# Kernel optimization log

Hardware: AMD Instinct MI355X
Metric: run time of the kernel (lower is better)

Reference implementation:

```python
import jax, jax.numpy as jnp
import numpy as np

B, GH, GW = 8, 32, 32
S = GH * GW            # 1024
HIDDEN = 512
D = 64                 # head_dim
NUM_HOPS = 2
EPS = 1e-6


def setup_inputs() -> dict:
    key = jax.random.key(0)
    ks = jax.random.split(key, 8)

    def init(k, shape, std):
        return (jax.random.normal(k, shape) * std).astype(jnp.float32)

    x = jax.random.normal(ks[0], (B, S, HIDDEN), dtype=jnp.float32)
    Wq = init(ks[1], (D, HIDDEN), HIDDEN ** -0.5)
    Wk = init(ks[2], (D, HIDDEN), HIDDEN ** -0.5)
    Wv = init(ks[3], (D, HIDDEN), HIDDEN ** -0.5)
    bias_table = init(ks[4], (2 * GH - 1, 2 * GW - 1), 0.02)
    fusion_w = jnp.ones((NUM_HOPS, 3), dtype=jnp.float32)
    fusion_b = jnp.zeros((NUM_HOPS,), dtype=jnp.float32)
    hop_W = init(ks[5], (NUM_HOPS, D, D), D ** -0.5)
    gate_W = init(ks[6], (NUM_HOPS, HIDDEN), HIDDEN ** -0.5)
    gate_b = jnp.zeros((NUM_HOPS,), dtype=jnp.float32)
    out_W = init(ks[7], (HIDDEN, D), D ** -0.5)
    temperature = jnp.ones((1,), dtype=jnp.float32)

    # relative position index [S, S] (buffer, constant)
    coords = np.stack(np.meshgrid(np.arange(GH), np.arange(GW), indexing='ij')).reshape(2, -1)
    rel = coords[:, :, None] - coords[:, None, :]
    rel[0] += GH - 1
    rel[1] += GW - 1
    rel_idx = jnp.asarray(rel[0] * (2 * GW - 1) + rel[1], dtype=jnp.int32)

    return dict(x=x, Wq=Wq, Wk=Wk, Wv=Wv, bias_table=bias_table,
                fusion_w=fusion_w, fusion_b=fusion_b, hop_W=hop_W,
                gate_W=gate_W, gate_b=gate_b, out_W=out_W,
                temperature=temperature, rel_idx=rel_idx)


def _rotate_half(u):
    d = u.shape[-1] // 2
    return jnp.concatenate([-u[..., d:], u[..., :d]], axis=-1)


def _prob_log(p):
    p = jnp.clip(p, EPS, 1.0 - EPS)
    return jnp.log(p / (1.0 - p + EPS))


def _mat_exp(M, h):
    R = M
    for _ in range(h - 1):
        R = jnp.matmul(R, M)
    return R


def _row_norm(M):
    return M / (jnp.sum(M, axis=-1, keepdims=True) + EPS)


def reference(x, Wq, Wk, Wv, bias_table, fusion_w, fusion_b, hop_W,
              gate_W, gate_b, out_W, temperature, rel_idx):
    b, s, hdim = x.shape
    d = Wq.shape[0]
    n_hops = hop_W.shape[0]
    scale = jnp.sqrt(jnp.float32(d))

    Q = jnp.einsum('bsh,dh->bsd', x, Wq)
    K = jnp.einsum('bsh,dh->bsd', x, Wk)
    V = jnp.einsum('bsh,dh->bsd', x, Wv)

    # RoPE (cached cos/sin are deterministic functions of S, D)
    inv_freq = 1.0 / (10000.0 ** (jnp.arange(0, d, 2, dtype=jnp.float32) / d))
    t = jnp.arange(s, dtype=jnp.float32)
    emb = jnp.concatenate([jnp.outer(t, inv_freq)] * 2, axis=-1)  # [S, D]
    cos, sin = jnp.cos(emb), jnp.sin(emb)
    Q = Q * cos + _rotate_half(Q) * sin
    K = K * cos + _rotate_half(K) * sin

    pb = bias_table.reshape(-1)[rel_idx]  # [S, S]
    scores = (jnp.einsum('bsd,btd->bst', Q, K) / scale + pb[None])
    scores = scores / jnp.clip(temperature, 0.1, None)
    A = jax.nn.softmax(scores, axis=-1)  # [B, S, S]

    A_T = jnp.swapaxes(A, -1, -2)
    AAt = jnp.matmul(A, A_T)
    AtA = jnp.matmul(A_T, A)

    hop_outs = []
    for hop in range(n_hops):
        h = hop + 1
        A_seq = _row_norm(_mat_exp(A, h))
        A_co = _row_norm(_mat_exp(AAt, h))
        A_sp = _row_norm(_mat_exp(AtA, h))
        fused_logit = (fusion_b[hop]
                       + fusion_w[hop, 0] * _prob_log(A_seq)
                       + fusion_w[hop, 1] * _prob_log(A_co)
                       + fusion_w[hop, 2] * _prob_log(A_sp))
        fused = _row_norm(jax.nn.sigmoid(fused_logit))
        hop_v = jnp.einsum('bsd,ed->bse', V, hop_W[hop])
        hop_outs.append(jnp.matmul(fused, hop_v))  # [B, S, D]

    gate = jax.nn.softmax(jnp.einsum('bsh,gh->bsg', x, gate_W) + gate_b, axis=-1)
    combined = sum(hop_outs[i] * gate[..., i:i + 1] for i in range(n_hops))
    return jnp.einsum('bsd,hd->bsh', combined, out_W)
```

## Files before the change

### kernel.cpp

```cpp
#include <hip/hip_runtime.h>
#include <hip/hip_bf16.h>

#define BB 8
#define SS 1024
#define HH 512
#define DD 64

typedef unsigned short u16;
typedef short v8s __attribute__((ext_vector_type(8)));
typedef float v4f __attribute__((ext_vector_type(4)));

__device__ __forceinline__ float bf2f(u16 u) {
    union { unsigned int i; float f; } v; v.i = ((unsigned int)u) << 16; return v.f;
}
__device__ __forceinline__ u16 f2bf(float f) {
    union { float f; unsigned int i; } v; v.f = f;
    unsigned int u = v.i;
    unsigned int r = u + 0x7fffu + ((u >> 16) & 1u);
    return (u16)(r >> 16);
}

__device__ __forceinline__ void gload16(const u16* g, u16* l) {
    __builtin_amdgcn_global_load_lds(
        (const __attribute__((address_space(1))) void*)g,
        (__attribute__((address_space(3))) void*)l,
        16, 0, 0);
}

__device__ __forceinline__ void tile_1024(
    const u16* __restrict__ Xb, const u16* __restrict__ Yb,
    u16* __restrict__ Cd, int tm, int tn, u16* Xs, u16* Ys, int mirror)
{
    int t = threadIdx.x, lane = t & 63, w = t >> 6;
    int wm = (w & 1) << 6, wn = (w >> 1) << 6;
    int fr = lane & 15, q = lane >> 4, m7 = fr & 7;
    int subrow = lane >> 3, cch = (lane & 7) ^ subrow;

    const u16* xg[4]; const u16* yg[4]; u16* xl[4]; u16* yl[4];
    #pragma unroll
    for (int i = 0; i < 4; i++) {
        int r = i * 32 + w * 8 + subrow;
        xg[i] = Xb + (long)(tm + r) * 1024 + cch * 8;
        yg[i] = Yb + (long)(tn + r) * 1024 + cch * 8;
        xl[i] = Xs + (i * 32 + w * 8) * 64;
        yl[i] = Ys + (i * 32 + w * 8) * 64;
    }

    v4f acc[4][4];
    #pragma unroll
    for (int i = 0; i < 4; i++)
        #pragma unroll
        for (int j = 0; j < 4; j++) {
            acc[i][j][0] = 0.f; acc[i][j][1] = 0.f; acc[i][j][2] = 0.f; acc[i][j][3] = 0.f;
        }

    for (int k0 = 0; k0 < 1024; k0 += 64) {
        __syncthreads();
        #pragma unroll
        for (int i = 0; i < 4; i++) { gload16(xg[i] + k0, xl[i]); gload16(yg[i] + k0, yl[i]); }
        __syncthreads();
        v8s af[2][4], bfr[2][4];
        #pragma unroll
        for (int h = 0; h < 2; h++) {
            int ca = (((h << 2) + q) ^ m7) << 3;
            #pragma unroll
            for (int s = 0; s < 4; s++) {
                af[h][s]  = *(const v8s*)(Xs + (wm + s * 16 + fr) * 64 + ca);
                bfr[h][s] = *(const v8s*)(Ys + (wn + s * 16 + fr) * 64 + ca);
            }
        }
        #pragma unroll
        for (int h = 0; h < 2; h++)
            #pragma unroll
            for (int i = 0; i < 4; i++)
                #pragma unroll
                for (int j = 0; j < 4; j++)
                    acc[i][j] = __builtin_amdgcn_mfma_f32_16x16x32_bf16(af[h][i], bfr[h][j], acc[i][j], 0, 0, 0);
    }
    #pragma unroll
    for (int i = 0; i < 4; i++) {
        int rowb = tm + wm + i * 16 + q * 4;
        #pragma unroll
        for (int j = 0; j < 4; j++) {
            int col = tn + wn + j * 16 + fr;
            ushort4 pv;
            pv.x = f2bf(acc[i][j][0]); pv.y = f2bf(acc[i][j][1]);
            pv.z = f2bf(acc[i][j][2]); pv.w = f2bf(acc[i][j][3]);
            #pragma unroll
            for (int r = 0; r < 4; r++)
                Cd[(long)(rowb + r) * 1024 + col] = ((u16*)&pv)[r];
            if (mirror)
                *(ushort4*)(Cd + (long)col * 1024 + rowb) = pv;
        }
    }
}

__device__ __forceinline__ void tile_k64(
    const u16* __restrict__ Xrows, const u16* __restrict__ Yrows,
    void* __restrict__ Cd, int crs, int cf32, u16* Xs, u16* Ys)
{
    int t = threadIdx.x, lane = t & 63, w = t >> 6;
    int wm = (w & 1) << 6, wn = (w >> 1) << 6;
    int fr = lane & 15, q = lane >> 4, m7 = fr & 7;
    int subrow = lane >> 3, cch = (lane & 7) ^ subrow;

    #pragma unroll
    for (int i = 0; i < 4; i++) {
        int r = i * 32 + w * 8 + subrow;
        gload16(Xrows + (long)r * 64 + cch * 8, Xs + (i * 32 + w * 8) * 64);
        gload16(Yrows + (long)r * 64 + cch * 8, Ys + (i * 32 + w * 8) * 64);
    }
    __syncthreads();

    v4f acc[4][4];
    #pragma unroll
    for (int i = 0; i < 4; i++)
        #pragma unroll
        for (int j = 0; j < 4; j++) {
            acc[i][j][0] = 0.f; acc[i][j][1] = 0.f; acc[i][j][2] = 0.f; acc[i][j][3] = 0.f;
        }
    v8s af[2][4], bfr[2][4];
    #pragma unroll
    for (int h = 0; h < 2; h++) {
        int ca = (((h << 2) + q) ^ m7) << 3;
        #pragma unroll
        for (int s = 0; s < 4; s++) {
            af[h][s]  = *(const v8s*)(Xs + (wm + s * 16 + fr) * 64 + ca);
            bfr[h][s] = *(const v8s*)(Ys + (wn + s * 16 + fr) * 64 + ca);
        }
    }
    #pragma unroll
    for (int h = 0; h < 2; h++)
        #pragma unroll
        for (int i = 0; i < 4; i++)
            #pragma unroll
            for (int j = 0; j < 4; j++)
                acc[i][j] = __builtin_amdgcn_mfma_f32_16x16x32_bf16(af[h][i], bfr[h][j], acc[i][j], 0, 0, 0);
    #pragma unroll
    for (int i = 0; i < 4; i++) {
        int rowb = wm + i * 16 + q * 4;
        #pragma unroll
        for (int j = 0; j < 4; j++) {
            int col = wn + j * 16 + fr;
            #pragma unroll
            for (int r = 0; r < 4; r++) {
                long o = (long)(rowb + r) * crs + col;
                if (cf32) ((float*)Cd)[o] = acc[i][j][r];
                else      ((u16*)Cd)[o] = f2bf(acc[i][j][r]);
            }
        }
    }
}

__device__ __forceinline__ void hop_tile(
    const u16* __restrict__ Fb, const u16* __restrict__ Hb,
    int y, int tmt, float* __restrict__ Pd, u16* Fs, u16* Hs)
{
    int tm = tmt * 128, kb = y * 256;
    int t = threadIdx.x, lane = t & 63, w = t >> 6;
    int fr = lane & 15, q = lane >> 4, m7 = fr & 7;
    int subrow = lane >> 3, cch = (lane & 7) ^ subrow;

    const u16* fg[4]; u16* fl[4]; const u16* hg[2]; u16* hl[2];
    #pragma unroll
    for (int i = 0; i < 4; i++) {
        int r = i * 32 + w * 8 + subrow;
        fg[i] = Fb + (long)(tm + r) * 1024 + cch * 8;
        fl[i] = Fs + (i * 32 + w * 8) * 64;
    }
    #pragma unroll
    for (int i = 0; i < 2; i++) {
        int r = i * 32 + w * 8 + subrow;
        hg[i] = Hb + (long)r * 1024 + cch * 8;
        hl[i] = Hs + (i * 32 + w * 8) * 64;
    }

    v4f acc[2][4];
    #pragma unroll
    for (int i = 0; i < 2; i++)
        #pragma unroll
        for (int j = 0; j < 4; j++) {
            acc[i][j][0] = 0.f; acc[i][j][1] = 0.f; acc[i][j][2] = 0.f; acc[i][j][3] = 0.f;
        }

    for (int k0 = kb; k0 < kb + 256; k0 += 64) {
        __syncthreads();
        #pragma unroll
        for (int i = 0; i < 4; i++) gload16(fg[i] + k0, fl[i]);
        #pragma unroll
        for (int i = 0; i < 2; i++) gload16(hg[i] + k0, hl[i]);
        __syncthreads();
        v8s af[2][2], bfr[2][4];
        #pragma unroll
        for (int h = 0; h < 2; h++) {
            int ca = (((h << 2) + q) ^ m7) << 3;
            #pragma unroll
            for (int s = 0; s < 2; s++)
                af[h][s] = *(const v8s*)(Fs + (w * 32 + s * 16 + fr) * 64 + ca);
            #pragma unroll
            for (int s = 0; s < 4; s++)
                bfr[h][s] = *(const v8s*)(Hs + (s * 16 + fr) * 64 + ca);
        }
        #pragma unroll
        for (int h = 0; h < 2; h++)
            #pragma unroll
            for (int i = 0; i < 2; i++)
                #pragma unroll
                for (int j = 0; j < 4; j++)
                    acc[i][j] = __builtin_amdgcn_mfma_f32_16x16x32_bf16(af[h][i], bfr[h][j], acc[i][j], 0, 0, 0);
    }
    #pragma unroll
    for (int i = 0; i < 2; i++) {
        int rowb = tm + w * 32 + i * 16 + q * 4;
        #pragma unroll
        for (int j = 0; j < 4; j++) {
            int col = j * 16 + fr;
            #pragma unroll
            for (int r = 0; r < 4; r++)
                Pd[(long)(rowb + r) * 64 + col] = acc[i][j][r];
        }
    }
}

__device__ __forceinline__ void fused_row(
    const u16* __restrict__ r1, const u16* __restrict__ r2, const u16* __restrict__ r3,
    float w0, float w1, float w2, float b0, u16* __restrict__ Frow, int lane)
{
    int base = lane << 4;
    union U { uint4 v; u16 s[8]; };
    U a[2], b[2], c[2];
    a[0].v = *(const uint4*)(r1 + base); a[1].v = *(const uint4*)(r1 + base + 8);
    b[0].v = *(const uint4*)(r2 + base); b[1].v = *(const uint4*)(r2 + base + 8);
    c[0].v = *(const uint4*)(r3 + base); c[1].v = *(const uint4*)(r3 + base + 8);
    float m1[16], m2[16], m3[16];
    float s1 = 0.f, s2 = 0.f, s3 = 0.f;
    #pragma unroll
    for (int h = 0; h < 2; h++)
        #pragma unroll
        for (int e = 0; e < 8; e++) {
            int k = h * 8 + e;
            m1[k] = bf2f(a[h].s[e]); m2[k] = bf2f(b[h].s[e]); m3[k] = bf2f(c[h].s[e]);
            s1 += m1[k]; s2 += m2[k]; s3 += m3[k];
        }
    #pragma unroll
    for (int o = 1; o < 64; o <<= 1) {
        s1 += __shfl_xor(s1, o); s2 += __shfl_xor(s2, o); s3 += __shfl_xor(s3, o);
    }
    float i1 = 1.f / (s1 + 1e-6f), i2 = 1.f / (s2 + 1e-6f), i3 = 1.f / (s3 + 1e-6f);
    float sig[16];
    float ssum = 0.f;
    #pragma unroll
    for (int k = 0; k < 16; k++) {
        float p1 = fminf(fmaxf(m1[k] * i1, 1e-6f), 1.0f - 1e-6f);
        float p2 = fminf(fmaxf(m2[k] * i2, 1e-6f), 1.0f - 1e-6f);
        float p3 = fminf(fmaxf(m3[k] * i3, 1e-6f), 1.0f - 1e-6f);
        float l1 = __logf(p1 / (1.0f - p1 + 1e-6f));
        float l2 = __logf(p2 / (1.0f - p2 + 1e-6f));
        float l3 = __logf(p3 / (1.0f - p3 + 1e-6f));
        float lg = b0 + w0 * l1 + w1 * l2 + w2 * l3;
        float sg = 1.0f / (1.0f + __expf(-lg));
        sig[k] = sg; ssum += sg;
    }
    #pragma unroll
    for (int o = 1; o < 64; o <<= 1) ssum += __shfl_xor(ssum, o);
    float inv = 1.0f / (ssum + 1e-6f);
    U o0, o1;
    #pragma unroll
    for (int e = 0; e < 8; e++) { o0.s[e] = f2bf(sig[e] * inv); o1.s[e] = f2bf(sig[8 + e] * inv); }
    *(uint4*)(Frow + base) = o0.v;
    *(uint4*)(Frow + base + 8) = o1.v;
}

__global__ __launch_bounds__(256) void gemm_link1(
    const u16* __restrict__ A, const u16* __restrict__ AT,
    u16* __restrict__ AAt, u16* __restrict__ AtA, u16* __restrict__ A2)
{
    __shared__ u16 Xs[128 * 64];
    __shared__ u16 Ys[128 * 64];
    const long SSq = (long)SS * SS;
    int b = blockIdx.x & 7;
    int job = blockIdx.x >> 3;
    const u16* Xb; const u16* Yb; u16* Cd;
    int ti, tj, mir;
    if (job < 72) {
        int tt = job < 36 ? job : job - 36;
        ti = 0;
        while (tt >= 8 - ti) { tt -= 8 - ti; ti++; }
        tj = ti + tt;
        mir = (ti != tj);
        if (job < 36) { Xb = A  + b * SSq; Yb = Xb; Cd = AAt + b * SSq; }
        else          { Xb = AT + b * SSq; Yb = Xb; Cd = AtA + b * SSq; }
    } else {
        int jj = job - 72;
        ti = jj >> 3; tj = jj & 7; mir = 0;
        Xb = A + b * SSq; Yb = AT + b * SSq; Cd = A2 + b * SSq;
    }
    tile_1024(Xb, Yb, Cd, ti * 128, tj * 128, Xs, Ys, mir);
}

__global__ __launch_bounds__(256) void gemm_link2h0(
    const u16* __restrict__ AAt, const u16* __restrict__ AtA,
    u16* __restrict__ AAt2, u16* __restrict__ AtA2,
    const u16* __restrict__ F0, const u16* __restrict__ hopVT,
    float* __restrict__ Pa, float* __restrict__ Pb)
{
    __shared__ u16 Xs[128 * 64];
    __shared__ u16 Ys[128 * 64];
    const long SSq = (long)SS * SS;
    int bx = blockIdx.x;
    if (bx < 576) {
        int z = bx & 15;
        int tt = bx >> 4, ti = 0;
        while (tt >= 8 - ti) { tt -= 8 - ti; ti++; }
        int tj = ti + tt;
        const u16* Xb = (z < 8 ? AAt : AtA) + (long)(z & 7) * SSq;
        u16* Cd = (z < 8 ? AAt2 : AtA2) + (long)(z & 7) * SSq;
        tile_1024(Xb, Xb, Cd, ti * 128, tj * 128, Xs, Ys, ti != tj);
    } else {
        int j = bx - 576;
        int y = j >> 6, rest = j & 63;
        int tmt = rest >> 3, b = rest & 7;
        float* Pd = (y < 2 ? Pa + (long)y * 16 * 65536 : Pb + (long)(y - 2) * 16 * 65536)
                    + (long)b * 65536;
        hop_tile(F0 + (long)b * SSq, hopVT + (long)b * 65536, y, tmt, Pd, Xs, Ys);
    }
}

__global__ __launch_bounds__(256) void gemm_hop1(
    const u16* __restrict__ F1, const u16* __restrict__ hopVT,
    float* __restrict__ Pa, float* __restrict__ Pb)
{
    __shared__ u16 Fs[128 * 64];
    __shared__ u16 Hs[64 * 64];
    const long SSq = (long)SS * SS;
    int j = blockIdx.x;
    int y = j >> 6, rest = j & 63;
    int tmt = rest >> 3, b = rest & 7;
    float* Pd = (y < 2 ? Pa + (long)y * 16 * 65536 : Pb + (long)(y - 2) * 16 * 65536)
                + (long)(8 + b) * 65536;
    hop_tile(F1 + (long)b * SSq, hopVT + (long)(8 + b) * 65536, y, tmt, Pd, Fs, Hs);
}

__global__ __launch_bounds__(256) void gemm_nt(
    const u16* __restrict__ X, long sx,
    const u16* __restrict__ Y, long sy,
    void* __restrict__ Cv, long sc,
    int M, int N, int K, int cf32)
{
    __shared__ u16 Xs[128 * 64];
    __shared__ u16 Ys[128 * 64];
    const u16* Xb = X + (long)blockIdx.z * sx;
    const u16* Yb = Y + (long)blockIdx.z * sy;
    int tm = blockIdx.x * 128, tn = blockIdx.y * 128;
    int t = threadIdx.x, lane = t & 63, w = t >> 6;
    int wm = (w & 1) << 6, wn = (w >> 1) << 6;
    int fr = lane & 15, q = lane >> 4, m7 = fr & 7;
    int subrow = lane >> 3, cch = (lane & 7) ^ subrow;

    const u16* xg[4]; const u16* yg[4]; u16* xl[4]; u16* yl[4];
    #pragma unroll
    for (int i = 0; i < 4; i++) {
        int r = i * 32 + w * 8 + subrow;
        xg[i] = Xb + (long)(tm + r) * K + cch * 8;
        yg[i] = Yb + (long)(tn + r) * K + cch * 8;
        xl[i] = Xs + (i * 32 + w * 8) * 64;
        yl[i] = Ys + (i * 32 + w * 8) * 64;
    }

    v4f acc[4][4];
    #pragma unroll
    for (int i = 0; i < 4; i++)
        #pragma unroll
        for (int j = 0; j < 4; j++) {
            acc[i][j][0] = 0.f; acc[i][j][1] = 0.f; acc[i][j][2] = 0.f; acc[i][j][3] = 0.f;
        }

    for (int k0 = 0; k0 < K; k0 += 64) {
        __syncthreads();
        #pragma unroll
        for (int i = 0; i < 4; i++) { gload16(xg[i] + k0, xl[i]); gload16(yg[i] + k0, yl[i]); }
        __syncthreads();
        v8s af[2][4], bfr[2][4];
        #pragma unroll
        for (int h = 0; h < 2; h++) {
            int ca = (((h << 2) + q) ^ m7) << 3;
            #pragma unroll
            for (int s = 0; s < 4; s++) {
                af[h][s]  = *(const v8s*)(Xs + (wm + s * 16 + fr) * 64 + ca);
                bfr[h][s] = *(const v8s*)(Ys + (wn + s * 16 + fr) * 64 + ca);
            }
        }
        #pragma unroll
        for (int h = 0; h < 2; h++)
            #pragma unroll
            for (int i = 0; i < 4; i++)
                #pragma unroll
                for (int j = 0; j < 4; j++)
                    acc[i][j] = __builtin_amdgcn_mfma_f32_16x16x32_bf16(af[h][i], bfr[h][j], acc[i][j], 0, 0, 0);
    }
    long cb = (long)blockIdx.z * sc;
    #pragma unroll
    for (int i = 0; i < 4; i++) {
        int rowb = tm + wm + i * 16 + q * 4;
        #pragma unroll
        for (int j = 0; j < 4; j++) {
            int col = tn + wn + j * 16 + fr;
            #pragma unroll
            for (int r = 0; r < 4; r++) {
                long o = cb + (long)(rowb + r) * N + col;
                if (cf32) ((float*)Cv)[o] = acc[i][j][r];
                else      ((u16*)Cv)[o] = f2bf(acc[i][j][r]);
            }
        }
    }
}

__global__ __launch_bounds__(256) void k_qk_hopv(
    const u16* __restrict__ Qb, const u16* __restrict__ Kb,
    const u16* __restrict__ Vb, const u16* __restrict__ hopWb,
    float* __restrict__ scores, u16* __restrict__ hopvC)
{
    __shared__ u16 Xs[128 * 64];
    __shared__ u16 Ys[128 * 64];
    const long SSq = (long)SS * SS;
    const long SD = (long)SS * DD;
    int bx = blockIdx.x;
    if (bx < 512) {
        int z = bx & 7;
        int tt = bx >> 3;
        int tm = (tt >> 3) * 128, tn = (tt & 7) * 128;
        tile_k64(Qb + z * SD + (long)tm * 64, Kb + z * SD + (long)tn * 64,
                 scores + z * SSq + (long)tm * 1024 + tn, 1024, 1, Xs, Ys);
    } else {
        int tm = (bx - 512) * 128;
        tile_k64(Vb + (long)tm * 64, hopWb,
                 hopvC + (long)tm * 128, 128, 0, Xs, Ys);
    }
}

__global__ __launch_bounds__(256) void k_sm_hvt(
    const float* __restrict__ scores, const float* __restrict__ btab,
    const float* __restrict__ temp, u16* __restrict__ A,
    const u16* __restrict__ hopvC, u16* __restrict__ hopVT)
{
    __shared__ __align__(16) float smf[3969];
    int bx = blockIdx.x;
    int t = threadIdx.x;
    if (bx < 2048) {
        for (int i = t; i < 3969; i += 256) smf[i] = btab[i];
        __syncthreads();
        int lane = t & 63, w = t >> 6;
        long row = (long)bx * 4 + w;
        int i = (int)(row & 1023);
        int ih = i >> 5, iw = i & 31;
        float inv_t = 1.0f / fmaxf(temp[0], 0.1f);
        const float* srow = scores + row * 1024;
        float sc[16];
        float m = -1e30f;
        #pragma unroll
        for (int c = 0; c < 16; c++) {
            int j = c * 64 + lane;
            int jh = j >> 5, jw = j & 31;
            float pb = smf[(ih - jh + 31) * 63 + (iw - jw + 31)];
            float s = (srow[j] * 0.125f + pb) * inv_t;
            sc[c] = s; m = fmaxf(m, s);
        }
        #pragma unroll
        for (int o = 1; o < 64; o <<= 1) m = fmaxf(m, __shfl_xor(m, o));
        float sum = 0.f;
        #pragma unroll
        for (int c = 0; c < 16; c++) { sc[c] = __expf(sc[c] - m); sum += sc[c]; }
        #pragma unroll
        for (int o = 1; o < 64; o <<= 1) sum += __shfl_xor(sum, o);
        float inv = 1.0f / sum;
        #pragma unroll
        for (int c = 0; c < 16; c++) A[row * 1024 + c * 64 + lane] = f2bf(sc[c] * inv);
    } else {
        u16* tile = (u16*)smf;
        int ex = bx - 2048;
        int hop = ex >> 7, rem = ex & 127;
        int z = rem & 7, i0 = (rem >> 3) * 64;
        const u16* s = hopvC + (long)z * (1024 * 128) + hop * 64;
        u16* d = hopVT + (long)(hop * 8 + z) * 65536;
        int r = t >> 2, c0 = (t & 3) << 4;
        #pragma unroll
        for (int p = 0; p < 2; p++) {
            int c = c0 + p * 8;
            uint4 v = *(const uint4*)(s + (long)(i0 + r) * 128 + c);
            *(uint4*)(&tile[r * 72 + c]) = v;
        }
        __syncthreads();
        #pragma unroll
        for (int p = 0; p < 2; p++) {
            uint4 ov; u16* po = (u16*)&ov;
            #pragma unroll
            for (int e = 0; e < 8; e++) po[e] = tile[(c0 + p * 8 + e) * 72 + r];
            *(uint4*)(d + (long)r * 1024 + i0 + c0 + p * 8) = ov;
        }
    }
}

__global__ __launch_bounds__(256) void k_fused0(
    const u16* __restrict__ A, const u16* __restrict__ AAt,
    const u16* __restrict__ AtA, const float* __restrict__ fw,
    const float* __restrict__ fbv, u16* __restrict__ F0)
{
    int lane = threadIdx.x & 63, w = threadIdx.x >> 6;
    float w0 = fw[0], w1 = fw[1], w2 = fw[2], b0 = fbv[0];
    long row = (long)blockIdx.x * 4 + w;
    fused_row(A + row * 1024, AAt + row * 1024, AtA + row * 1024,
              w0, w1, w2, b0, F0 + row * 1024, lane);
}

__global__ __launch_bounds__(256) void k_fused1(
    const u16* __restrict__ A2, const u16* __restrict__ AAt2,
    const u16* __restrict__ AtA2, const float* __restrict__ fw,
    const float* __restrict__ fbv, u16* __restrict__ F1)
{
    int lane = threadIdx.x & 63, w = threadIdx.x >> 6;
    float w0 = fw[3], w1 = fw[4], w2 = fw[5], b0 = fbv[1];
    long row = (long)blockIdx.x * 4 + w;
    fused_row(A2 + row * 1024, AAt2 + row * 1024, AtA2 + row * 1024,
              w0, w1, w2, b0, F1 + row * 1024, lane);
}

__global__ __launch_bounds__(256) void k_pack(
    const float* __restrict__ x, const float* __restrict__ Wq,
    const float* __restrict__ Wk, const float* __restrict__ Wv,
    const float* __restrict__ gW, const float* __restrict__ hopW,
    const float* __restrict__ outW, u16* __restrict__ xb,
    u16* __restrict__ wpack, u16* __restrict__ hopWb, u16* __restrict__ outWb)
{
    int bx = blockIdx.x;
    if (bx < 4096) {
        long i = (long)bx * 256 + threadIdx.x;
        float4 v = ((const float4*)x)[i];
        ushort4 o;
        o.x = f2bf(v.x); o.y = f2bf(v.y); o.z = f2bf(v.z); o.w = f2bf(v.w);
        ((ushort4*)xb)[i] = o;
    } else {
        int idx = (bx - 4096) * 256 + threadIdx.x;
        if (idx < 131072) {
            int r = idx >> 9, c = idx & 511;
            float v = 0.f;
            if (r < 64)       v = Wq[r * 512 + c];
            else if (r < 128) v = Wk[(r - 64) * 512 + c];
            else if (r < 192) v = Wv[(r - 128) * 512 + c];
            else if (r < 194) v = gW[(r - 192) * 512 + c];
            wpack[idx] = f2bf(v);
        } else if (idx < 131072 + 8192) {
            int i = idx - 131072;
            hopWb[i] = f2bf(hopW[i]);
        } else if (idx < 131072 + 8192 + 32768) {
            int i = idx - 131072 - 8192;
            outWb[i] = f2bf(outW[i]);
        }
    }
}

__global__ __launch_bounds__(256) void k_rope(
    const float* __restrict__ QKVG, const float* __restrict__ gateb,
    u16* __restrict__ Qb, u16* __restrict__ Kb, u16* __restrict__ Vb,
    float* __restrict__ gate)
{
    int t = threadIdx.x, l = t & 63, w = t >> 6;
    long row = (long)blockIdx.x * 4 + w;
    int spos = (int)(row & (SS - 1));
    const float* base = QKVG + row * 256;
    float q = base[l], k = base[64 + l], v = base[128 + l];
    float qp = __shfl_xor(q, 32), kp = __shfl_xor(k, 32);
    float sgn = (l < 32) ? -1.f : 1.f;
    int f = l & 31;
    float ang = (float)spos * exp2f(-(float)f * (13.287712379549449f / 32.0f));
    float cs = cosf(ang), sn = sinf(ang);
    Qb[row * 64 + l] = f2bf(q * cs + sgn * qp * sn);
    Kb[row * 64 + l] = f2bf(k * cs + sgn * kp * sn);
    Vb[row * 64 + l] = f2bf(v);
    if (l < 2) {
        float g0 = base[192] + gateb[0], g1 = base[193] + gateb[1];
        float m = fmaxf(g0, g1);
        float e0 = __expf(g0 - m), e1 = __expf(g1 - m);
        gate[row * 2 + l] = ((l == 0) ? e0 : e1) / (e0 + e1);
    }
}

__global__ __launch_bounds__(256) void k_transpose(
    const u16* __restrict__ src, u16* __restrict__ dst,
    int srs, int drs, long sbs, long dbs)
{
    __shared__ u16 tile[64 * 72];
    const u16* s = src + (long)blockIdx.z * sbs;
    u16* d = dst + (long)blockIdx.z * dbs;
    int i0 = blockIdx.x * 64, j0 = blockIdx.y * 64;
    int t = threadIdx.x;
    int r = t >> 2, c0 = (t & 3) << 4;
    #pragma unroll
    for (int p = 0; p < 2; p++) {
        int c = c0 + p * 8;
        uint4 v = *(const uint4*)(s + (long)(i0 + r) * srs + j0 + c);
        *(uint4*)(&tile[r * 72 + c]) = v;
    }
    __syncthreads();
    #pragma unroll
    for (int p = 0; p < 2; p++) {
        uint4 ov;
        u16* po = (u16*)&ov;
        #pragma unroll
        for (int e = 0; e < 8; e++) po[e] = tile[(c0 + p * 8 + e) * 72 + r];
        *(uint4*)(d + (long)(j0 + r) * drs + i0 + c0 + p * 8) = ov;
    }
}

__global__ __launch_bounds__(256) void k_combine(
    const float* __restrict__ Pa, const float* __restrict__ Pb,
    const float* __restrict__ gate, u16* __restrict__ comb)
{
    long idx = (long)blockIdx.x * 256 + threadIdx.x;
    long srow = idx >> 6;
    int b = (int)(srow >> 10);
    long o = (long)(srow & 1023) * 64 + (idx & 63);
    float h0 = Pa[(long)b * 65536 + o] + Pa[(long)(16 + b) * 65536 + o]
             + Pb[(long)b * 65536 + o] + Pb[(long)(16 + b) * 65536 + o];
    float h1 = Pa[(long)(8 + b) * 65536 + o] + Pa[(long)(24 + b) * 65536 + o]
             + Pb[(long)(8 + b) * 65536 + o] + Pb[(long)(24 + b) * 65536 + o];
    float g0 = gate[srow * 2], g1 = gate[srow * 2 + 1];
    comb[idx] = f2bf(h0 * g0 + h1 * g1);
}

extern "C" void kernel_launch(void* const* d_in, const int* in_sizes, int n_in,
                              void* d_out, int out_size, void* d_ws, size_t ws_size,
                              hipStream_t stream) {
    const float* x    = (const float*)d_in[0];
    const float* Wq   = (const float*)d_in[1];
    const float* Wk   = (const float*)d_in[2];
    const float* Wv   = (const float*)d_in[3];
    const float* btab = (const float*)d_in[4];
    const float* fw   = (const float*)d_in[5];
    const float* fbv  = (const float*)d_in[6];
    const float* hopW = (const float*)d_in[7];
    const float* gW   = (const float*)d_in[8];
    const float* gb   = (const float*)d_in[9];
    const float* outW = (const float*)d_in[10];
    const float* temp = (const float*)d_in[11];
    float* out = (float*)d_out;

    char* wsb = (char*)d_ws;
    size_t off = 0;
    auto take = [&](size_t n) { char* p = wsb + off; off += (n + 255) & ~(size_t)255; return p; };
    u16* Qb      = (u16*)take(8192L * 64 * 2);
    u16* Kb      = (u16*)take(8192L * 64 * 2);
    u16* Vb      = (u16*)take(8192L * 64 * 2);
    float* gate  = (float*)take(8192L * 2 * 4);
    u16* wpack   = (u16*)take(256L * 512 * 2);
    u16* hopWb   = (u16*)take(2L * 64 * 64 * 2);
    u16* outWb   = (u16*)take(512L * 64 * 2);
    u16* hopvC   = (u16*)take(8192L * 128 * 2);
    u16* hopVT   = (u16*)take(2L * 8 * 64 * 1024 * 2);
    float* Pa    = (float*)take(2L * 16 * 65536 * 4);
    u16* comb    = (u16*)take(8192L * 64 * 2);
    float* scoresF = (float*)take(8L * 1024 * 1024 * 4);
    float* QKVG  = (float*)scoresF;
    u16* F0      = (u16*)scoresF;
    u16* F1      = (u16*)scoresF + 8L * 1024 * 1024;
    u16* A       = (u16*)take(8L * 1024 * 1024 * 2);
    u16* xb      = (u16*)A;
    u16* AT      = (u16*)take(8L * 1024 * 1024 * 2);
    float* Pb    = (float*)AT;
    u16* AAt     = (u16*)take(8L * 1024 * 1024 * 2);
    u16* AtA     = (u16*)take(8L * 1024 * 1024 * 2);
    u16* A2      = (u16*)take(8L * 1024 * 1024 * 2);
    u16* AAt2    = (u16*)take(8L * 1024 * 1024 * 2);
    u16* AtA2    = (u16*)take(8L * 1024 * 1024 * 2);
    (void)ws_size; (void)in_sizes; (void)n_in; (void)out_size;

    const long SSq = (long)SS * SS;

    k_pack<<<4768, 256, 0, stream>>>(x, Wq, Wk, Wv, gW, hopW, outW, xb, wpack, hopWb, outWb);
    gemm_nt<<<dim3(64, 2, 1), 256, 0, stream>>>(xb, 0, wpack, 0, QKVG, 0, 8192, 256, 512, 1);
    k_rope<<<2048, 256, 0, stream>>>(QKVG, gb, Qb, Kb, Vb, gate);
    k_qk_hopv<<<576, 256, 0, stream>>>(Qb, Kb, Vb, hopWb, scoresF, hopvC);
    k_sm_hvt<<<2304, 256, 0, stream>>>(scoresF, btab, temp, A, hopvC, hopVT);
    k_transpose<<<dim3(16, 16, 8), 256, 0, stream>>>(A, AT, 1024, 1024, SSq, SSq);
    gemm_link1<<<1088, 256, 0, stream>>>(A, AT, AAt, AtA, A2);
    k_fused0<<<2048, 256, 0, stream>>>(A, AAt, AtA, fw, fbv, F0);
    gemm_link2h0<<<832, 256, 0, stream>>>(AAt, AtA, AAt2, AtA2, F0, hopVT, Pa, Pb);
    k_fused1<<<2048, 256, 0, stream>>>(A2, AAt2, AtA2, fw, fbv, F1);
    gemm_hop1<<<256, 256, 0, stream>>>(F1, hopVT, Pa, Pb);
    k_combine<<<2048, 256, 0, stream>>>(Pa, Pb, gate, comb);
    gemm_nt<<<dim3(64, 4, 1), 256, 0, stream>>>(comb, 0, outWb, 0, out, 0, 8192, 512, 64, 1);
}
```

Baseline: 305.1 us.

## Fuse projection with RoPE, softmax with transpose, and regroup stages

Moves the RoPE, V and gate-softmax epilogue into the QKV projection GEMM. It reads cos/sin from a table precomputed in the pack kernel, so the fp32 QKVG intermediate and the k_rope launch go away. The softmax kernel now also writes A transposed through shared memory, which removes the separate transpose pass. The fused-logit row kernels are regrouped into the same launches as independent GEMMs (link2 with fused0, hop0 with fused1), cutting launches and overlapping bandwidth-bound and compute-bound work. The cost is more shared memory in the softmax kernel and scattered 8-byte transposed stores.

```diff
diff --git a/kernel.cpp b/kernel.cpp
--- a/kernel.cpp
+++ b/kernel.cpp
@@ -298,11 +298,11 @@
     tile_1024(Xb, Yb, Cd, ti * 128, tj * 128, Xs, Ys, mir);
 }
 
-__global__ __launch_bounds__(256) void gemm_link2h0(
+__global__ __launch_bounds__(256) void k_link2_fused0(
     const u16* __restrict__ AAt, const u16* __restrict__ AtA,
     u16* __restrict__ AAt2, u16* __restrict__ AtA2,
-    const u16* __restrict__ F0, const u16* __restrict__ hopVT,
-    float* __restrict__ Pa, float* __restrict__ Pb)
+    const u16* __restrict__ A, const float* __restrict__ fw,
+    const float* __restrict__ fbv, u16* __restrict__ F0)
 {
     __shared__ u16 Xs[128 * 64];
     __shared__ u16 Ys[128 * 64];
@@ -317,12 +317,37 @@
         u16* Cd = (z < 8 ? AAt2 : AtA2) + (long)(z & 7) * SSq;
         tile_1024(Xb, Xb, Cd, ti * 128, tj * 128, Xs, Ys, ti != tj);
     } else {
-        int j = bx - 576;
-        int y = j >> 6, rest = j & 63;
+        int lane = threadIdx.x & 63, w = threadIdx.x >> 6;
+        float w0 = fw[0], w1 = fw[1], w2 = fw[2], b0 = fbv[0];
+        long row = (long)(bx - 576) * 4 + w;
+        fused_row(A + row * 1024, AAt + row * 1024, AtA + row * 1024,
+                  w0, w1, w2, b0, F0 + row * 1024, lane);
+    }
+}
+
+__global__ __launch_bounds__(256) void k_hop0_fused1(
+    const u16* __restrict__ F0, const u16* __restrict__ hopVT,
+    float* __restrict__ Pa, float* __restrict__ Pb,
+    const u16* __restrict__ A2, const u16* __restrict__ AAt2,
+    const u16* __restrict__ AtA2, const float* __restrict__ fw,
+    const float* __restrict__ fbv, u16* __restrict__ F1)
+{
+    __shared__ u16 Fs[128 * 64];
+    __shared__ u16 Hs[64 * 64];
+    const long SSq = (long)SS * SS;
+    int bx = blockIdx.x;
+    if (bx < 256) {
+        int y = bx >> 6, rest = bx & 63;
         int tmt = rest >> 3, b = rest & 7;
         float* Pd = (y < 2 ? Pa + (long)y * 16 * 65536 : Pb + (long)(y - 2) * 16 * 65536)
                     + (long)b * 65536;
-        hop_tile(F0 + (long)b * SSq, hopVT + (long)b * 65536, y, tmt, Pd, Xs, Ys);
+        hop_tile(F0 + (long)b * SSq, hopVT + (long)b * 65536, y, tmt, Pd, Fs, Hs);
+    } else {
+        int lane = threadIdx.x & 63, w = threadIdx.x >> 6;
+        float w0 = fw[3], w1 = fw[4], w2 = fw[5], b0 = fbv[1];
+        long row = (long)(bx - 256) * 4 + w;
+        fused_row(A2 + row * 1024, AAt2 + row * 1024, AtA2 + row * 1024,
+                  w0, w1, w2, b0, F1 + row * 1024, lane);
     }
 }
 
@@ -412,6 +437,108 @@
                 else      ((u16*)Cv)[o] = f2bf(acc[i][j][r]);
             }
         }
+    }
+}
+
+__global__ __launch_bounds__(256) void k_proj_rope(
+    const u16* __restrict__ xb, const u16* __restrict__ wpack,
+    const float* __restrict__ gateb, const float2* __restrict__ ropetab,
+    u16* __restrict__ Qb, u16* __restrict__ Kb, u16* __restrict__ Vb,
+    float* __restrict__ gate)
+{
+    __shared__ u16 Xs[128 * 64];
+    __shared__ u16 Ys[128 * 64];
+    int tm = blockIdx.x * 128, tn = blockIdx.y * 128;
+    int t = threadIdx.x, lane = t & 63, w = t >> 6;
+    int wm = (w & 1) << 6, wn = (w >> 1) << 6;
+    int fr = lane & 15, q = lane >> 4, m7 = fr & 7;
+    int subrow = lane >> 3, cch = (lane & 7) ^ subrow;
+
+    const u16* xg[4]; const u16* yg[4]; u16* xl[4]; u16* yl[4];
+    #pragma unroll
+    for (int i = 0; i < 4; i++) {
+        int r = i * 32 + w * 8 + subrow;
+        xg[i] = xb + (long)(tm + r) * 512 + cch * 8;
+        yg[i] = wpack + (long)(tn + r) * 512 + cch * 8;
+        xl[i] = Xs + (i * 32 + w * 8) * 64;
+        yl[i] = Ys + (i * 32 + w * 8) * 64;
+    }
+
+    v4f acc[4][4];
+    #pragma unroll
+    for (int i = 0; i < 4; i++)
+        #pragma unroll
+        for (int j = 0; j < 4; j++) {
+            acc[i][j][0] = 0.f; acc[i][j][1] = 0.f; acc[i][j][2] = 0.f; acc[i][j][3] = 0.f;
+        }
+
+    for (int k0 = 0; k0 < 512; k0 += 64) {
+        __syncthreads();
+        #pragma unroll
+        for (int i = 0; i < 4; i++) { gload16(xg[i] + k0, xl[i]); gload16(yg[i] + k0, yl[i]); }
+        __syncthreads();
+        v8s af[2][4], bfr[2][4];
+        #pragma unroll
+        for (int h = 0; h < 2; h++) {
+            int ca = (((h << 2) + q) ^ m7) << 3;
+            #pragma unroll
+            for (int s = 0; s < 4; s++) {
+                af[h][s]  = *(const v8s*)(Xs + (wm + s * 16 + fr) * 64 + ca);
+                bfr[h][s] = *(const v8s*)(Ys + (wn + s * 16 + fr) * 64 + ca);
+            }
+        }
+        #pragma unroll
+        for (int h = 0; h < 2; h++)
+            #pragma unroll
+            for (int i = 0; i < 4; i++)
+                #pragma unroll
+                for (int j = 0; j < 4; j++)
+                    acc[i][j] = __builtin_amdgcn_mfma_f32_16x16x32_bf16(af[h][i], bfr[h][j], acc[i][j], 0, 0, 0);
+    }
+
+    if (blockIdx.y == 0) {
+        u16* dst = wn ? Kb : Qb;
+        #pragma unroll
+        for (int i = 0; i < 4; i++) {
+            #pragma unroll
+            for (int r = 0; r < 4; r++) {
+                int row = tm + wm + i * 16 + q * 4 + r;
+                int spos = row & (SS - 1);
+                float2 t0 = ropetab[spos * 32 + fr];
+                float2 t1 = ropetab[spos * 32 + 16 + fr];
+                #pragma unroll
+                for (int j = 0; j < 4; j++) {
+                    float v = acc[i][j][r], p = acc[i][j ^ 2][r];
+                    float cs = (j & 1) ? t1.x : t0.x;
+                    float sn = (j & 1) ? t1.y : t0.y;
+                    float o = (j & 2) ? (v * cs + p * sn) : (v * cs - p * sn);
+                    dst[(long)row * 64 + j * 16 + fr] = f2bf(o);
+                }
+            }
+        }
+    } else if (wn == 0) {
+        #pragma unroll
+        for (int i = 0; i < 4; i++)
+            #pragma unroll
+            for (int j = 0; j < 4; j++)
+                #pragma unroll
+                for (int r = 0; r < 4; r++) {
+                    int row = tm + wm + i * 16 + q * 4 + r;
+                    Vb[(long)row * 64 + j * 16 + fr] = f2bf(acc[i][j][r]);
+                }
+    } else {
+        float gb = gateb[fr & 1];
+        #pragma unroll
+        for (int i = 0; i < 4; i++)
+            #pragma unroll
+            for (int r = 0; r < 4; r++) {
+                int row = tm + wm + i * 16 + q * 4 + r;
+                float g = acc[i][0][r] + gb;
+                float go = __shfl_xor(g, 1);
+                float m = fmaxf(g, go);
+                float e = __expf(g - m), eo = __expf(go - m);
+                if (fr < 2) gate[(long)row * 2 + fr] = e / (e + eo);
+            }
     }
 }
 
@@ -441,9 +568,11 @@
 __global__ __launch_bounds__(256) void k_sm_hvt(
     const float* __restrict__ scores, const float* __restrict__ btab,
     const float* __restrict__ temp, u16* __restrict__ A,
+    u16* __restrict__ AT,
     const u16* __restrict__ hopvC, u16* __restrict__ hopVT)
 {
     __shared__ __align__(16) float smf[3969];
+    __shared__ __align__(8) u16 Atile[4096];
     int bx = blockIdx.x;
     int t = threadIdx.x;
     if (bx < 2048) {
@@ -474,7 +603,24 @@
         for (int o = 1; o < 64; o <<= 1) sum += __shfl_xor(sum, o);
         float inv = 1.0f / sum;
         #pragma unroll
-        for (int c = 0; c < 16; c++) A[row * 1024 + c * 64 + lane] = f2bf(sc[c] * inv);
+        for (int c = 0; c < 16; c++) {
+            u16 bv = f2bf(sc[c] * inv);
+            A[row * 1024 + c * 64 + lane] = bv;
+            Atile[w * 1024 + c * 64 + lane] = bv;
+        }
+        __syncthreads();
+        int row0 = bx * 4;
+        int bb = row0 >> 10;
+        int i0 = row0 & 1023;
+        u16* ATb = AT + (long)bb * ((long)SS * SS);
+        #pragma unroll
+        for (int k = 0; k < 4; k++) {
+            int col = k * 256 + t;
+            ushort4 ov;
+            ov.x = Atile[col];        ov.y = Atile[1024 + col];
+            ov.z = Atile[2048 + col]; ov.w = Atile[3072 + col];
+            *(ushort4*)(ATb + (long)col * 1024 + i0) = ov;
+        }
     } else {
         u16* tile = (u16*)smf;
         int ex = bx - 2048;
@@ -500,36 +646,13 @@
     }
 }
 
-__global__ __launch_bounds__(256) void k_fused0(
-    const u16* __restrict__ A, const u16* __restrict__ AAt,
-    const u16* __restrict__ AtA, const float* __restrict__ fw,
-    const float* __restrict__ fbv, u16* __restrict__ F0)
-{
-    int lane = threadIdx.x & 63, w = threadIdx.x >> 6;
-    float w0 = fw[0], w1 = fw[1], w2 = fw[2], b0 = fbv[0];
-    long row = (long)blockIdx.x * 4 + w;
-    fused_row(A + row * 1024, AAt + row * 1024, AtA + row * 1024,
-              w0, w1, w2, b0, F0 + row * 1024, lane);
-}
-
-__global__ __launch_bounds__(256) void k_fused1(
-    const u16* __restrict__ A2, const u16* __restrict__ AAt2,
-    const u16* __restrict__ AtA2, const float* __restrict__ fw,
-    const float* __restrict__ fbv, u16* __restrict__ F1)
-{
-    int lane = threadIdx.x & 63, w = threadIdx.x >> 6;
-    float w0 = fw[3], w1 = fw[4], w2 = fw[5], b0 = fbv[1];
-    long row = (long)blockIdx.x * 4 + w;
-    fused_row(A2 + row * 1024, AAt2 + row * 1024, AtA2 + row * 1024,
-              w0, w1, w2, b0, F1 + row * 1024, lane);
-}
-
 __global__ __launch_bounds__(256) void k_pack(
     const float* __restrict__ x, const float* __restrict__ Wq,
     const float* __restrict__ Wk, const float* __restrict__ Wv,
     const float* __restrict__ gW, const float* __restrict__ hopW,
     const float* __restrict__ outW, u16* __restrict__ xb,
-    u16* __restrict__ wpack, u16* __restrict__ hopWb, u16* __restrict__ outWb)
+    u16* __restrict__ wpack, u16* __restrict__ hopWb, u16* __restrict__ outWb,
+    float2* __restrict__ ropetab)
 {
     int bx = blockIdx.x;
     if (bx < 4096) {
@@ -538,7 +661,7 @@
         ushort4 o;
         o.x = f2bf(v.x); o.y = f2bf(v.y); o.z = f2bf(v.z); o.w = f2bf(v.w);
         ((ushort4*)xb)[i] = o;
-    } else {
+    } else if (bx < 4768) {
         int idx = (bx - 4096) * 256 + threadIdx.x;
         if (idx < 131072) {
             int r = idx >> 9, c = idx & 511;
@@ -555,59 +678,13 @@
             int i = idx - 131072 - 8192;
             outWb[i] = f2bf(outW[i]);
         }
-    }
-}
-
-__global__ __launch_bounds__(256) void k_rope(
-    const float* __restrict__ QKVG, const float* __restrict__ gateb,
-    u16* __restrict__ Qb, u16* __restrict__ Kb, u16* __restrict__ Vb,
-    float* __restrict__ gate)
-{
-    int t = threadIdx.x, l = t & 63, w = t >> 6;
-    long row = (long)blockIdx.x * 4 + w;
-    int spos = (int)(row & (SS - 1));
-    const float* base = QKVG + row * 256;
-    float q = base[l], k = base[64 + l], v = base[128 + l];
-    float qp = __shfl_xor(q, 32), kp = __shfl_xor(k, 32);
-    float sgn = (l < 32) ? -1.f : 1.f;
-    int f = l & 31;
-    float ang = (float)spos * exp2f(-(float)f * (13.287712379549449f / 32.0f));
-    float cs = cosf(ang), sn = sinf(ang);
-    Qb[row * 64 + l] = f2bf(q * cs + sgn * qp * sn);
-    Kb[row * 64 + l] = f2bf(k * cs + sgn * kp * sn);
-    Vb[row * 64 + l] = f2bf(v);
-    if (l < 2) {
-        float g0 = base[192] + gateb[0], g1 = base[193] + gateb[1];
-        float m = fmaxf(g0, g1);
-        float e0 = __expf(g0 - m), e1 = __expf(g1 - m);
-        gate[row * 2 + l] = ((l == 0) ? e0 : e1) / (e0 + e1);
-    }
-}
-
-__global__ __launch_bounds__(256) void k_transpose(
-    const u16* __restrict__ src, u16* __restrict__ dst,
-    int srs, int drs, long sbs, long dbs)
-{
-    __shared__ u16 tile[64 * 72];
-    const u16* s = src + (long)blockIdx.z * sbs;
-    u16* d = dst + (long)blockIdx.z * dbs;
-    int i0 = blockIdx.x * 64, j0 = blockIdx.y * 64;
-    int t = threadIdx.x;
-    int r = t >> 2, c0 = (t & 3) << 4;
-    #pragma unroll
-    for (int p = 0; p < 2; p++) {
-        int c = c0 + p * 8;
-        uint4 v = *(const uint4*)(s + (long)(i0 + r) * srs + j0 + c);
-        *(uint4*)(&tile[r * 72 + c]) = v;
-    }
-    __syncthreads();
-    #pragma unroll
-    for (int p = 0; p < 2; p++) {
-        uint4 ov;
-        u16* po = (u16*)&ov;
-        #pragma unroll
-        for (int e = 0; e < 8; e++) po[e] = tile[(c0 + p * 8 + e) * 72 + r];
-        *(uint4*)(d + (long)(j0 + r) * drs + i0 + c0 + p * 8) = ov;
+    } else {
+        int idx = (bx - 4768) * 256 + threadIdx.x;
+        int spos = idx >> 5, f = idx & 31;
+        float ang = (float)spos * exp2f(-(float)f * (13.287712379549449f / 32.0f));
+        float sn, cs;
+        sincosf(ang, &sn, &cs);
+        ropetab[idx] = make_float2(cs, sn);
     }
 }
 
@@ -654,12 +731,12 @@
     u16* wpack   = (u16*)take(256L * 512 * 2);
     u16* hopWb   = (u16*)take(2L * 64 * 64 * 2);
     u16* outWb   = (u16*)take(512L * 64 * 2);
+    float2* ropetab = (float2*)take(1024L * 32 * 8);
     u16* hopvC   = (u16*)take(8192L * 128 * 2);
     u16* hopVT   = (u16*)take(2L * 8 * 64 * 1024 * 2);
     float* Pa    = (float*)take(2L * 16 * 65536 * 4);
     u16* comb    = (u16*)take(8192L * 64 * 2);
     float* scoresF = (float*)take(8L * 1024 * 1024 * 4);
-    float* QKVG  = (float*)scoresF;
     u16* F0      = (u16*)scoresF;
     u16* F1      = (u16*)scoresF + 8L * 1024 * 1024;
     u16* A       = (u16*)take(8L * 1024 * 1024 * 2);
@@ -673,18 +750,16 @@
     u16* AtA2    = (u16*)take(8L * 1024 * 1024 * 2);
     (void)ws_size; (void)in_sizes; (void)n_in; (void)out_size;
 
-    const long SSq = (long)SS * SS;
-
-    k_pack<<<4768, 256, 0, stream>>>(x, Wq, Wk, Wv, gW, hopW, outW, xb, wpack, hopWb, outWb);
-    gemm_nt<<<dim3(64, 2, 1), 256, 0, stream>>>(xb, 0, wpack, 0, QKVG, 0, 8192, 256, 512, 1);
-    k_rope<<<2048, 256, 0, stream>>>(QKVG, gb, Qb, Kb, Vb, gate);
+    k_pack<<<4896, 256, 0, stream>>>(x, Wq, Wk, Wv, gW, hopW, outW, xb, wpack,
+                                     hopWb, outWb, ropetab);
+    k_proj_rope<<<dim3(64, 2, 1), 256, 0, stream>>>(xb, wpack, gb, ropetab,
+                                                    Qb, Kb, Vb, gate);
     k_qk_hopv<<<576, 256, 0, stream>>>(Qb, Kb, Vb, hopWb, scoresF, hopvC);
-    k_sm_hvt<<<2304, 256, 0, stream>>>(scoresF, btab, temp, A, hopvC, hopVT);
-    k_transpose<<<dim3(16, 16, 8), 256, 0, stream>>>(A, AT, 1024, 1024, SSq, SSq);
+    k_sm_hvt<<<2304, 256, 0, stream>>>(scoresF, btab, temp, A, AT, hopvC, hopVT);
     gemm_link1<<<1088, 256, 0, stream>>>(A, AT, AAt, AtA, A2);
-    k_fused0<<<2048, 256, 0, stream>>>(A, AAt, AtA, fw, fbv, F0);
-    gemm_link2h0<<<832, 256, 0, stream>>>(AAt, AtA, AAt2, AtA2, F0, hopVT, Pa, Pb);
-    k_fused1<<<2048, 256, 0, stream>>>(A2, AAt2, AtA2, fw, fbv, F1);
+    k_link2_fused0<<<2624, 256, 0, stream>>>(AAt, AtA, AAt2, AtA2, A, fw, fbv, F0);
+    k_hop0_fused1<<<2304, 256, 0, stream>>>(F0, hopVT, Pa, Pb, A2, AAt2, AtA2,
+                                            fw, fbv, F1);
     gemm_hop1<<<256, 256, 0, stream>>>(F1, hopVT, Pa, Pb);
     k_combine<<<2048, 256, 0, stream>>>(Pa, Pb, gate, comb);
     gemm_nt<<<dim3(64, 4, 1), 256, 0, stream>>>(comb, 0, outWb, 0, out, 0, 8192, 512, 64, 1);
```

After: 301.7 us. No clear change (-1.1%).
